# Optimization experiments

Measured on AMD Instinct MI355X. Metric: run time of the kernel, lower is better.

## Reference

```python
import jax, jax.numpy as jnp
import numpy as np
import itertools

B, N, IN_DIM, H_DIM, OUT_DIM, K = 64, 32, 128, 512, 256, 2


def _uniform(key, shape, fan_in):
    bound = 1.0 / np.sqrt(fan_in)
    return jax.random.uniform(key, shape, jnp.float32, -bound, bound)


def setup_inputs() -> dict:
    key = jax.random.key(0)
    ks = jax.random.split(key, 7)
    x = jax.random.normal(ks[0], (B, N, IN_DIM), jnp.float32)
    W1 = _uniform(ks[1], (IN_DIM * K, H_DIM), IN_DIM * K)
    b1 = _uniform(ks[2], (H_DIM,), IN_DIM * K)
    W2 = _uniform(ks[3], (H_DIM, H_DIM), H_DIM)
    b2 = _uniform(ks[4], (H_DIM,), H_DIM)
    W3 = _uniform(ks[5], (H_DIM, OUT_DIM), H_DIM)
    b3 = _uniform(ks[6], (OUT_DIM,), H_DIM)
    return {"x": x, "W1": W1, "b1": b1, "W2": W2, "b2": b2, "W3": W3, "b3": b3}


def reference(x, W1, b1, W2, b2, W3, b3):
    n = x.shape[1]
    # all k-permutations of set indices, itertools order: [P, K], P = N*(N-1) for K=2
    perm = jnp.asarray(np.array(list(itertools.permutations(range(n), K)), dtype=np.int32))
    # gather: [B, P, K, in_dim] -> flatten last two dims -> [B, P, K*in_dim]
    xp = x[:, perm, :].reshape(x.shape[0], perm.shape[0], K * x.shape[2])
    h = jax.nn.relu(jnp.einsum('bpf,fh->bph', xp, W1) + b1)
    h = jax.nn.relu(jnp.einsum('bph,hg->bpg', h, W2) + b2)
    out = jnp.einsum('bpg,go->bpo', h, W3) + b3
    return out.sum(axis=1)  # sum over permutations -> [B, out_dim]
```

## Files before the change

kernel.cpp:

```cpp
#include <hip/hip_runtime.h>

#define BB 64
#define NN 32
#define IND 128
#define HD 512
#define OD 256
#define NPERM 992

typedef __attribute__((ext_vector_type(8))) _Float16 half8;
typedef __attribute__((ext_vector_type(4))) _Float16 half4;
typedef __attribute__((ext_vector_type(16))) float f32x16;

typedef __attribute__((address_space(3))) char lds_char_t;
typedef __attribute__((address_space(1))) const char gbl_char_t;

__device__ __forceinline__ void glds16(const void* g, void* l) {
    __builtin_amdgcn_global_load_lds((gbl_char_t*)g, (lds_char_t*)l, 16, 0, 0);
}

#define WAITVM8 asm volatile("s_waitcnt vmcnt(8)" ::: "memory")
#define WAITVM0 asm volatile("s_waitcnt vmcnt(0)" ::: "memory")
#define RBAR __builtin_amdgcn_s_barrier()

__device__ __forceinline__ half8 relu8(half8 x) {
    half8 z = 0;
    return __builtin_elementwise_max(x, z);
}

#define XTO 69632
__global__ __launch_bounds__(512, 4) void kprep(
    const float* __restrict__ x, const float* __restrict__ W1, const float* __restrict__ b1,
    const float* __restrict__ W2, _Float16* __restrict__ W2t,
    const float* __restrict__ b3, float* __restrict__ out,
    _Float16* __restrict__ U, _Float16* __restrict__ Vo) {
    __shared__ char smem[(256 + 32) * 272];
    const int bid = blockIdx.x;
    const int t = threadIdx.x;

    if (bid >= 256) {
        const int bid2 = bid - 256;
        float (*tile)[65] = (float (*)[65])smem;
        if (t < 256) out[(size_t)bid2 * OD + t] = (float)NPERM * b3[t];
        const int k0 = (bid2 & 7) * 64, c0 = (bid2 >> 3) * 64;
        const int cin = t & 63, r0 = (t >> 6) * 8;
#pragma unroll
        for (int rr = 0; rr < 8; ++rr)
            tile[r0 + rr][cin] = W2[(size_t)(k0 + r0 + rr) * HD + c0 + cin];
        __syncthreads();
        const int kout = t & 63;
#pragma unroll
        for (int rr = 0; rr < 8; ++rr) {
            int c = r0 + rr;
            W2t[(size_t)(c0 + c) * HD + k0 + kout] = (_Float16)tile[kout][c];
        }
        return;
    }

    const int g = bid & 3, b = bid >> 2;
    const int h0 = (g & 1) * 256;
    const int koff = (g >> 1) * 128;

    {
        const int n = t >> 4, c8 = (t & 15) * 8;
        const float* src = x + ((size_t)(b * NN + n)) * IND + c8;
        float4 f0 = *(const float4*)src;
        float4 f1 = *(const float4*)(src + 4);
        half8 h;
        h[0] = (_Float16)f0.x; h[1] = (_Float16)f0.y;
        h[2] = (_Float16)f0.z; h[3] = (_Float16)f0.w;
        h[4] = (_Float16)f1.x; h[5] = (_Float16)f1.y;
        h[6] = (_Float16)f1.z; h[7] = (_Float16)f1.w;
        *(half8*)(smem + XTO + n * 272 + c8 * 2) = h;
    }
    {
        const int ht = t & 63, ktb = t >> 6;
#pragma unroll
        for (int it = 0; it < 4; ++it) {
            const int kt = ktb + it * 8;
            const float* wsrc = W1 + (size_t)(koff + kt * 4) * HD + h0 + ht * 4;
            float4 v0 = *(const float4*)(wsrc);
            float4 v1 = *(const float4*)(wsrc + HD);
            float4 v2 = *(const float4*)(wsrc + 2 * HD);
            float4 v3 = *(const float4*)(wsrc + 3 * HD);
            char* wdst = smem + (size_t)(ht * 4) * 272 + kt * 8;
            half4 o0 = {(_Float16)v0.x, (_Float16)v1.x, (_Float16)v2.x, (_Float16)v3.x};
            half4 o1 = {(_Float16)v0.y, (_Float16)v1.y, (_Float16)v2.y, (_Float16)v3.y};
            half4 o2 = {(_Float16)v0.z, (_Float16)v1.z, (_Float16)v2.z, (_Float16)v3.z};
            half4 o3 = {(_Float16)v0.w, (_Float16)v1.w, (_Float16)v2.w, (_Float16)v3.w};
            *(half4*)(wdst) = o0;
            *(half4*)(wdst + 272) = o1;
            *(half4*)(wdst + 544) = o2;
            *(half4*)(wdst + 816) = o3;
        }
    }
    __syncthreads();

    const int lane = t & 63, wv = t >> 6;
    const int l31 = lane & 31, hi = lane >> 5;
    const char* abase = smem + XTO + (size_t)l31 * 272 + hi * 16;
    const char* bbase = smem + (size_t)(wv * 32 + l31) * 272 + hi * 16;

    f32x16 acc;
#pragma unroll
    for (int r = 0; r < 16; ++r) acc[r] = 0.f;
#pragma unroll
    for (int ks = 0; ks < 8; ++ks) {
        half8 a  = *(const half8*)(abase + ks * 32);
        half8 bf = *(const half8*)(bbase + ks * 32);
        acc = __builtin_amdgcn_mfma_f32_32x32x16_f16(a, bf, acc, 0, 0, 0);
    }
    const int hglob = h0 + wv * 32 + l31;
    const float bias = (g < 2) ? b1[hglob] : 0.f;
    _Float16* dst = ((g < 2) ? U : Vo) + (size_t)b * NN * HD + hglob;
#pragma unroll
    for (int r = 0; r < 16; ++r) {
        int row = (r & 3) + 8 * (r >> 2) + 4 * hi;
        dst[(size_t)row * HD] = (_Float16)(acc[r] + bias);
    }
}

#define VOFF 65536
#define UOFF 98304
__global__ __launch_bounds__(512, 2) void k2(
    const _Float16* __restrict__ Ug, const _Float16* __restrict__ Vg,
    const _Float16* __restrict__ W2t, const float* __restrict__ b2,
    const float* __restrict__ W3, float* __restrict__ out) {
    __shared__ char smb[131072];
    __shared__ float red[8][64];
    __shared__ float hred[64];

    const int b = blockIdx.x;
    const int cb0 = blockIdx.y * 64;
    const int t = threadIdx.x;
    const int lane = t & 63, wid = t >> 6;
    const int l31 = lane & 31, hi = lane >> 5;
    const int lh = lane >> 5, lm = lane & 31;
    const unsigned sw = (unsigned)((l31 & 15) << 4);

#pragma unroll
    for (int h = 0; h < 2; ++h) {
#pragma unroll
        for (int ii = 0; ii < 4; ++ii) {
            int r = wid * 8 + ii * 2 + lh;
            const char* src = (const char*)W2t + (size_t)(cb0 + r) * 1024 + h * 512
                              + ((lm * 16) ^ ((r & 15) << 4));
            glds16(src, smb + h * 32768 + (wid * 8 + ii * 2) * 512);
        }
#pragma unroll
        for (int ii = 0; ii < 2; ++ii) {
            int r = wid * 4 + ii * 2 + lh;
            const char* src = (const char*)Ug + (size_t)(b * NN + r) * 1024 + h * 512 + lm * 16;
            glds16(src, smb + UOFF + h * 16384 + (wid * 4 + ii * 2) * 512);
        }
#pragma unroll
        for (int ii = 0; ii < 2; ++ii) {
            int r = wid * 4 + ii * 2 + lh;
            const char* src = (const char*)Vg + (size_t)(b * NN + r) * 1024 + h * 512
                              + ((lm * 16) ^ ((r & 15) << 4));
            glds16(src, smb + VOFF + h * 16384 + (wid * 4 + ii * 2) * 512);
        }
    }
    WAITVM8;
    RBAR;

    f32x16 acc[4][2];
#pragma unroll
    for (int rf = 0; rf < 4; ++rf)
#pragma unroll
        for (int cf = 0; cf < 2; ++cf)
#pragma unroll
            for (int r = 0; r < 16; ++r) acc[rf][cf][r] = 0.f;

#pragma unroll
    for (int kh = 0; kh < 2; ++kh) {
        const unsigned ub = (unsigned)(UOFF + kh * 16384 + wid * 4 * 512 + hi * 16);
        const unsigned vb = (unsigned)(VOFF + kh * 16384 + l31 * 512);
        const unsigned b0b = (unsigned)(kh * 32768 + l31 * 512);
        const unsigned b1b = (unsigned)(kh * 32768 + (32 + l31) * 512);

        half8 pU0, pU1, pU2, pU3, pV, pB0, pB1;
        {
            unsigned kx = ((unsigned)(hi * 16)) ^ sw;
            pU0 = *(const half8*)(smb + ub + 0 * 512);
            pU1 = *(const half8*)(smb + ub + 1 * 512);
            pU2 = *(const half8*)(smb + ub + 2 * 512);
            pU3 = *(const half8*)(smb + ub + 3 * 512);
            pV  = *(const half8*)(smb + vb + kx);
            pB0 = *(const half8*)(smb + b0b + kx);
            pB1 = *(const half8*)(smb + b1b + kx);
        }
#pragma unroll
        for (int kk = 0; kk < 16; ++kk) {
            half8 cU0 = pU0, cU1 = pU1, cU2 = pU2, cU3 = pU3;
            half8 cV = pV, cB0 = pB0, cB1 = pB1;
            if (kk < 15) {
                int kn = kk + 1;
                unsigned kx = ((unsigned)(kn * 32 + hi * 16)) ^ sw;
                pU0 = *(const half8*)(smb + ub + 0 * 512 + kn * 32);
                pU1 = *(const half8*)(smb + ub + 1 * 512 + kn * 32);
                pU2 = *(const half8*)(smb + ub + 2 * 512 + kn * 32);
                pU3 = *(const half8*)(smb + ub + 3 * 512 + kn * 32);
                pV  = *(const half8*)(smb + vb + kx);
                pB0 = *(const half8*)(smb + b0b + kx);
                pB1 = *(const half8*)(smb + b1b + kx);
            }

            half8 af0 = relu8(cU0 + cV);
            half8 af1 = relu8(cU1 + cV);
            half8 af2 = relu8(cU2 + cV);
            half8 af3 = relu8(cU3 + cV);

            __builtin_amdgcn_s_setprio(1);
            acc[0][0] = __builtin_amdgcn_mfma_f32_32x32x16_f16(af0, cB0, acc[0][0], 0, 0, 0);
            acc[0][1] = __builtin_amdgcn_mfma_f32_32x32x16_f16(af0, cB1, acc[0][1], 0, 0, 0);
            acc[1][0] = __builtin_amdgcn_mfma_f32_32x32x16_f16(af1, cB0, acc[1][0], 0, 0, 0);
            acc[1][1] = __builtin_amdgcn_mfma_f32_32x32x16_f16(af1, cB1, acc[1][1], 0, 0, 0);
            acc[2][0] = __builtin_amdgcn_mfma_f32_32x32x16_f16(af2, cB0, acc[2][0], 0, 0, 0);
            acc[2][1] = __builtin_amdgcn_mfma_f32_32x32x16_f16(af2, cB1, acc[2][1], 0, 0, 0);
            acc[3][0] = __builtin_amdgcn_mfma_f32_32x32x16_f16(af3, cB0, acc[3][0], 0, 0, 0);
            acc[3][1] = __builtin_amdgcn_mfma_f32_32x32x16_f16(af3, cB1, acc[3][1], 0, 0, 0);
            __builtin_amdgcn_s_setprio(0);
        }
        if (kh == 0) {
            WAITVM0;
            RBAR;
        }
    }

    float scf[2];
#pragma unroll
    for (int cf = 0; cf < 2; ++cf) {
        int col = cb0 + cf * 32 + l31;
        float b2v = b2[col];
        float s = 0.f;
#pragma unroll
        for (int rf = 0; rf < 4; ++rf) {
            int i_idx = wid * 4 + rf;
#pragma unroll
            for (int r = 0; r < 16; ++r) {
                int row = (r & 3) + 8 * (r >> 2) + 4 * hi;
                float h2 = fmaxf(acc[rf][cf][r] + b2v, 0.f);
                if (row != i_idx) s += h2;
            }
        }
        s += __shfl_xor(s, 32);
        scf[cf] = s;
    }
    if (lane < 32) {
        red[wid][l31] = scf[0];
        red[wid][32 + l31] = scf[1];
    }
    __syncthreads();

    if (t < 64) {
        float hsum = 0.f;
#pragma unroll
        for (int w = 0; w < 8; ++w) hsum += red[w][t];
        hred[t] = hsum;
    }
    __syncthreads();

    {
        int o = t & 255, gg = t >> 8;
        const float* w3p = W3 + ((size_t)(cb0 + gg * 32)) * OD + o;
        float a = 0.f;
#pragma unroll 8
        for (int j = 0; j < 32; ++j)
            a += hred[gg * 32 + j] * w3p[(size_t)j * OD];
        atomicAdd(&out[(size_t)b * OD + o], a);
    }
}

extern "C" void kernel_launch(void* const* d_in, const int* in_sizes, int n_in,
                              void* d_out, int out_size, void* d_ws, size_t ws_size,
                              hipStream_t stream) {
    const float* x  = (const float*)d_in[0];
    const float* W1 = (const float*)d_in[1];
    const float* b1 = (const float*)d_in[2];
    const float* W2 = (const float*)d_in[3];
    const float* b2 = (const float*)d_in[4];
    const float* W3 = (const float*)d_in[5];
    const float* b3 = (const float*)d_in[6];
    float* out = (float*)d_out;

    _Float16* U   = (_Float16*)d_ws;
    _Float16* V   = U + (size_t)BB * NN * HD;
    _Float16* W2t = V + (size_t)BB * NN * HD;

    hipLaunchKernelGGL(kprep, dim3(320), dim3(512), 0, stream,
                       x, W1, b1, W2, W2t, b3, out, U, V);
    hipLaunchKernelGGL(k2, dim3(64, 8), dim3(512), 0, stream, U, V, W2t, b2, W3, out);
}
```

Baseline: 43.33 us.

## Process two batches per k2 block with double-buffered U/V prefetch

Result: no change. 42.60 us (-1.7%).

```diff
diff --git a/kernel.cpp b/kernel.cpp
--- a/kernel.cpp
+++ b/kernel.cpp
@@ -19,7 +19,10 @@
 }
 
 #define WAITVM8 asm volatile("s_waitcnt vmcnt(8)" ::: "memory")
+#define WAITVM4 asm volatile("s_waitcnt vmcnt(4)" ::: "memory")
+#define WAITVM1 asm volatile("s_waitcnt vmcnt(1)" ::: "memory")
 #define WAITVM0 asm volatile("s_waitcnt vmcnt(0)" ::: "memory")
+#define WAITLGKM asm volatile("s_waitcnt lgkmcnt(0)" ::: "memory")
 #define RBAR __builtin_amdgcn_s_barrier()
 
 __device__ __forceinline__ half8 relu8(half8 x) {
@@ -119,8 +122,8 @@
     }
 }
 
-#define VOFF 65536
-#define UOFF 98304
+#define SLOT0 65536
+#define SLOT1 98304
 __global__ __launch_bounds__(512, 2) void k2(
     const _Float16* __restrict__ Ug, const _Float16* __restrict__ Vg,
     const _Float16* __restrict__ W2t, const float* __restrict__ b2,
@@ -129,7 +132,7 @@
     __shared__ float red[8][64];
     __shared__ float hred[64];
 
-    const int b = blockIdx.x;
+    const int bp = blockIdx.x;
     const int cb0 = blockIdx.y * 64;
     const int t = threadIdx.x;
     const int lane = t & 63, wid = t >> 6;
@@ -137,46 +140,54 @@
     const int lh = lane >> 5, lm = lane & 31;
     const unsigned sw = (unsigned)((l31 & 15) << 4);
 
-#pragma unroll
-    for (int h = 0; h < 2; ++h) {
+    auto issueB = [&](int kh) {
 #pragma unroll
         for (int ii = 0; ii < 4; ++ii) {
             int r = wid * 8 + ii * 2 + lh;
-            const char* src = (const char*)W2t + (size_t)(cb0 + r) * 1024 + h * 512
+            const char* src = (const char*)W2t + (size_t)(cb0 + r) * 1024 + kh * 512
                               + ((lm * 16) ^ ((r & 15) << 4));
-            glds16(src, smb + h * 32768 + (wid * 8 + ii * 2) * 512);
-        }
+            glds16(src, smb + kh * 32768 + (wid * 8 + ii * 2) * 512);
+        }
+    };
+    auto issueUV = [&](int bb, int kh, unsigned slotOff) {
 #pragma unroll
         for (int ii = 0; ii < 2; ++ii) {
             int r = wid * 4 + ii * 2 + lh;
-            const char* src = (const char*)Ug + (size_t)(b * NN + r) * 1024 + h * 512 + lm * 16;
-            glds16(src, smb + UOFF + h * 16384 + (wid * 4 + ii * 2) * 512);
+            const char* src = (const char*)Vg + (size_t)(bb * NN + r) * 1024 + kh * 512
+                              + ((lm * 16) ^ ((r & 15) << 4));
+            glds16(src, smb + slotOff + (wid * 4 + ii * 2) * 512);
         }
 #pragma unroll
         for (int ii = 0; ii < 2; ++ii) {
             int r = wid * 4 + ii * 2 + lh;
-            const char* src = (const char*)Vg + (size_t)(b * NN + r) * 1024 + h * 512
-                              + ((lm * 16) ^ ((r & 15) << 4));
-            glds16(src, smb + VOFF + h * 16384 + (wid * 4 + ii * 2) * 512);
-        }
-    }
+            const char* src = (const char*)Ug + (size_t)(bb * NN + r) * 1024 + kh * 512 + lm * 16;
+            glds16(src, smb + slotOff + 16384 + (wid * 4 + ii * 2) * 512);
+        }
+    };
+
+    const int bA = bp * 2, bB = bp * 2 + 1;
+    issueB(0);
+    issueUV(bA, 0, SLOT0);
+    issueB(1);
+    issueUV(bA, 1, SLOT1);
     WAITVM8;
     RBAR;
 
     f32x16 acc[4][2];
-#pragma unroll
-    for (int rf = 0; rf < 4; ++rf)
-#pragma unroll
-        for (int cf = 0; cf < 2; ++cf)
-#pragma unroll
-            for (int r = 0; r < 16; ++r) acc[rf][cf][r] = 0.f;
-
-#pragma unroll
-    for (int kh = 0; kh < 2; ++kh) {
-        const unsigned ub = (unsigned)(UOFF + kh * 16384 + wid * 4 * 512 + hi * 16);
-        const unsigned vb = (unsigned)(VOFF + kh * 16384 + l31 * 512);
-        const unsigned b0b = (unsigned)(kh * 32768 + l31 * 512);
-        const unsigned b1b = (unsigned)(kh * 32768 + (32 + l31) * 512);
+    auto resetAcc = [&]() {
+#pragma unroll
+        for (int rf = 0; rf < 4; ++rf)
+#pragma unroll
+            for (int cf = 0; cf < 2; ++cf)
+#pragma unroll
+                for (int r = 0; r < 16; ++r) acc[rf][cf][r] = 0.f;
+    };
+
+    auto compute = [&](unsigned slotOff, int kh) {
+        const unsigned ub = slotOff + 16384u + (unsigned)(wid * 4 * 512) + (unsigned)(hi * 16);
+        const unsigned vb = slotOff + (unsigned)(l31 * 512);
+        const unsigned bb0 = (unsigned)(kh * 32768 + l31 * 512);
+        const unsigned bb1 = (unsigned)(kh * 32768 + (32 + l31) * 512);
 
         half8 pU0, pU1, pU2, pU3, pV, pB0, pB1;
         {
@@ -186,8 +197,8 @@
             pU2 = *(const half8*)(smb + ub + 2 * 512);
             pU3 = *(const half8*)(smb + ub + 3 * 512);
             pV  = *(const half8*)(smb + vb + kx);
-            pB0 = *(const half8*)(smb + b0b + kx);
-            pB1 = *(const half8*)(smb + b1b + kx);
+            pB0 = *(const half8*)(smb + bb0 + kx);
+            pB1 = *(const half8*)(smb + bb1 + kx);
         }
 #pragma unroll
         for (int kk = 0; kk < 16; ++kk) {
@@ -201,8 +212,8 @@
                 pU2 = *(const half8*)(smb + ub + 2 * 512 + kn * 32);
                 pU3 = *(const half8*)(smb + ub + 3 * 512 + kn * 32);
                 pV  = *(const half8*)(smb + vb + kx);
-                pB0 = *(const half8*)(smb + b0b + kx);
-                pB1 = *(const half8*)(smb + b1b + kx);
+                pB0 = *(const half8*)(smb + bb0 + kx);
+                pB1 = *(const half8*)(smb + bb1 + kx);
             }
 
             half8 af0 = relu8(cU0 + cV);
@@ -221,54 +232,69 @@
             acc[3][1] = __builtin_amdgcn_mfma_f32_32x32x16_f16(af3, cB1, acc[3][1], 0, 0, 0);
             __builtin_amdgcn_s_setprio(0);
         }
-        if (kh == 0) {
-            WAITVM0;
-            RBAR;
-        }
-    }
-
-    float scf[2];
-#pragma unroll
-    for (int cf = 0; cf < 2; ++cf) {
-        int col = cb0 + cf * 32 + l31;
-        float b2v = b2[col];
-        float s = 0.f;
-#pragma unroll
-        for (int rf = 0; rf < 4; ++rf) {
-            int i_idx = wid * 4 + rf;
-#pragma unroll
-            for (int r = 0; r < 16; ++r) {
-                int row = (r & 3) + 8 * (r >> 2) + 4 * hi;
-                float h2 = fmaxf(acc[rf][cf][r] + b2v, 0.f);
-                if (row != i_idx) s += h2;
+    };
+
+    auto sums_gemv = [&]() -> float {
+        float scf[2];
+#pragma unroll
+        for (int cf = 0; cf < 2; ++cf) {
+            int col = cb0 + cf * 32 + l31;
+            float b2v = b2[col];
+            float s = 0.f;
+#pragma unroll
+            for (int rf = 0; rf < 4; ++rf) {
+                int i_idx = wid * 4 + rf;
+#pragma unroll
+                for (int r = 0; r < 16; ++r) {
+                    int row = (r & 3) + 8 * (r >> 2) + 4 * hi;
+                    float h2 = fmaxf(acc[rf][cf][r] + b2v, 0.f);
+                    if (row != i_idx) s += h2;
+                }
             }
-        }
-        s += __shfl_xor(s, 32);
-        scf[cf] = s;
-    }
-    if (lane < 32) {
-        red[wid][l31] = scf[0];
-        red[wid][32 + l31] = scf[1];
-    }
-    __syncthreads();
-
-    if (t < 64) {
-        float hsum = 0.f;
-#pragma unroll
-        for (int w = 0; w < 8; ++w) hsum += red[w][t];
-        hred[t] = hsum;
-    }
-    __syncthreads();
-
-    {
+            s += __shfl_xor(s, 32);
+            scf[cf] = s;
+        }
+        if (lane < 32) {
+            red[wid][l31] = scf[0];
+            red[wid][32 + l31] = scf[1];
+        }
+        WAITLGKM; RBAR;
+        if (t < 64) {
+            float hsum = 0.f;
+#pragma unroll
+            for (int w = 0; w < 8; ++w) hsum += red[w][t];
+            hred[t] = hsum;
+        }
+        WAITLGKM; RBAR;
         int o = t & 255, gg = t >> 8;
         const float* w3p = W3 + ((size_t)(cb0 + gg * 32)) * OD + o;
         float a = 0.f;
 #pragma unroll 8
         for (int j = 0; j < 32; ++j)
             a += hred[gg * 32 + j] * w3p[(size_t)j * OD];
-        atomicAdd(&out[(size_t)b * OD + o], a);
-    }
+        return a;
+    };
+
+    resetAcc();
+    compute(SLOT0, 0);
+    RBAR;
+    issueUV(bB, 0, SLOT0);
+    WAITVM4;
+    RBAR;
+    compute(SLOT1, 1);
+    RBAR;
+    issueUV(bB, 1, SLOT1);
+    float a0 = sums_gemv();
+    WAITVM4;
+    atomicAdd(&out[(size_t)bA * OD + (t & 255)], a0);
+    RBAR;
+    resetAcc();
+    compute(SLOT0, 0);
+    WAITVM1;
+    RBAR;
+    compute(SLOT1, 1);
+    float a1 = sums_gemv();
+    atomicAdd(&out[(size_t)bB * OD + (t & 255)], a1);
 }
 
 extern "C" void kernel_launch(void* const* d_in, const int* in_sizes, int n_in,
@@ -289,5 +315,5 @@
 
     hipLaunchKernelGGL(kprep, dim3(320), dim3(512), 0, stream,
                        x, W1, b1, W2, W2t, b3, out, U, V);
-    hipLaunchKernelGGL(k2, dim3(64, 8), dim3(512), 0, stream, U, V, W2t, b2, W3, out);
-}
+    hipLaunchKernelGGL(k2, dim3(32, 8), dim3(512), 0, stream, U, V, W2t, b2, W3, out);
+}
```
